# Optimization experiments

Measured on AMD Instinct MI355X. Metric: run time of the kernel, lower is better.

The kernel has to match this reference:

```python
import jax, jax.numpy as jnp
import numpy as np

NODE_DIM = 128
CAT = 16
N_NODES = 100000
N_EDGES = 200000
N_SCALARS = 6
INPUT_DIM = 5 * NODE_DIM + 5 * CAT + N_SCALARS  # 726
CELL_H, NET_H, OUT = 192, 128, 128
EPS = 1e-5


def setup_inputs() -> dict:
    key = jax.random.key(0)
    ks = jax.random.split(key, 24)
    inp = {
        'h_nodes': jax.random.normal(ks[0], (N_NODES, NODE_DIM), jnp.float32),
        'edge_scalars': jax.random.normal(ks[1], (N_EDGES, N_SCALARS), jnp.float32),
        'edge_src': jax.random.randint(ks[2], (N_EDGES,), 0, N_NODES),
        'edge_dst': jax.random.randint(ks[3], (N_EDGES,), 0, N_NODES),
        'edge_type': jax.random.randint(ks[4], (N_EDGES,), 0, 2),
        'cell_type_src': jax.random.randint(ks[5], (N_EDGES,), 0, 256),
        'cell_type_dst': jax.random.randint(ks[6], (N_EDGES,), 0, 256),
        'pin_role_src': jax.random.randint(ks[7], (N_EDGES,), 0, 64),
        'pin_role_dst': jax.random.randint(ks[8], (N_EDGES,), 0, 64),
        # embedding tables
        'emb_edge_type': jax.random.normal(ks[9], (2, CAT), jnp.float32),
        'emb_cell_type': jax.random.normal(ks[10], (256, CAT), jnp.float32),
        'emb_pin_role': jax.random.normal(ks[11], (64, CAT), jnp.float32),
        # cell MLP params
        'cell_W1': jax.random.normal(ks[12], (INPUT_DIM, CELL_H), jnp.float32) * (1.0 / np.sqrt(INPUT_DIM)),
        'cell_b1': jnp.zeros((CELL_H,), jnp.float32),
        'cell_g': jnp.ones((CELL_H,), jnp.float32),
        'cell_beta': jnp.zeros((CELL_H,), jnp.float32),
        'cell_W2': jax.random.normal(ks[13], (CELL_H, OUT), jnp.float32) * (1.0 / np.sqrt(CELL_H)),
        'cell_b2': jnp.zeros((OUT,), jnp.float32),
        # net MLP params
        'net_W1': jax.random.normal(ks[14], (INPUT_DIM, NET_H), jnp.float32) * (1.0 / np.sqrt(INPUT_DIM)),
        'net_b1': jnp.zeros((NET_H,), jnp.float32),
        'net_g': jnp.ones((NET_H,), jnp.float32),
        'net_beta': jnp.zeros((NET_H,), jnp.float32),
        'net_W2': jax.random.normal(ks[15], (NET_H, OUT), jnp.float32) * (1.0 / np.sqrt(NET_H)),
        'net_b2': jnp.zeros((OUT,), jnp.float32),
    }
    return inp


def _oov(x, n):
    return jnp.where((x >= 0) & (x < n), x, 0)


def _mlp(x, W1, b1, g, beta, W2, b2):
    h = x @ W1 + b1
    mu = jnp.mean(h, axis=-1, keepdims=True)
    var = jnp.mean(jnp.square(h - mu), axis=-1, keepdims=True)
    h = (h - mu) * jax.lax.rsqrt(var + EPS) * g + beta
    h = jax.nn.relu(h)
    return h @ W2 + b2


def reference(h_nodes, edge_scalars, emb_edge_type, emb_cell_type, emb_pin_role,
              cell_W1, cell_b1, cell_g, cell_beta, cell_W2, cell_b2,
              net_W1, net_b1, net_g, net_beta, net_W2, net_b2,
              edge_src, edge_dst, edge_type, cell_type_src, cell_type_dst,
              pin_role_src, pin_role_dst):
    h_u = h_nodes[edge_src]                      # [E, D]
    h_v = h_nodes[edge_dst]
    h_prod = h_u * h_v
    h_abs_diff = jnp.abs(h_u - h_v)
    h_signed_diff = h_v - h_u
    e_et = emb_edge_type[_oov(edge_type, emb_edge_type.shape[0])]
    e_ct_s = emb_cell_type[_oov(cell_type_src, emb_cell_type.shape[0])]
    e_ct_d = emb_cell_type[_oov(cell_type_dst, emb_cell_type.shape[0])]
    e_pr_s = emb_pin_role[_oov(pin_role_src, emb_pin_role.shape[0])]
    e_pr_d = emb_pin_role[_oov(pin_role_dst, emb_pin_role.shape[0])]
    scal = jnp.clip(edge_scalars, -10.0, 10.0)
    feat = jnp.concatenate([h_u, h_v, h_prod, h_abs_diff, h_signed_diff,
                            e_et, e_ct_s, e_ct_d, e_pr_s, e_pr_d, scal], axis=-1)  # [E, 726]
    out_cell = _mlp(feat, cell_W1, cell_b1, cell_g, cell_beta, cell_W2, cell_b2)
    out_net = _mlp(feat, net_W1, net_b1, net_g, net_beta, net_W2, net_b2)
    et = edge_type[:, None]
    h_edges = jnp.where(et == 0, out_cell, jnp.where(et == 1, out_net, jnp.zeros_like(out_cell)))
    return h_edges
```

## Files before the change

kernel.cpp:

```cpp
#include <hip/hip_runtime.h>

#define KPAD 736
#define KS   23
#define FPAD 744
#define BM   32

typedef short bfrag8 __attribute__((ext_vector_type(8)));
typedef float f32x4 __attribute__((ext_vector_type(4)));

__device__ __forceinline__ unsigned short f2bf(float f) {
  union { float f; unsigned u; } v; v.f = f;
  unsigned r = v.u + 0x7fffu + ((v.u >> 16) & 1u);
  return (unsigned short)(r >> 16);
}
__device__ __forceinline__ unsigned pk2(float a, float b) {
  return (unsigned)f2bf(a) | ((unsigned)f2bf(b) << 16);
}

struct SmemP2 {
  unsigned short hb[BM][200];
  float red[4][BM][2];
  float mu[BM];
  float rs[BM];
  float ot[BM][132];
};
struct alignas(16) Smem {
  union {
    unsigned short feat[BM][FPAD];
    SmemP2 p2;
  } u;
};

__global__ void prep_weights(const float* __restrict__ cW1, const float* __restrict__ nW1,
                             const float* __restrict__ cW2, const float* __restrict__ nW2,
                             unsigned short* __restrict__ w1c, unsigned short* __restrict__ w1n,
                             unsigned short* __restrict__ w2c, unsigned short* __restrict__ w2n,
                             int* __restrict__ cnt) {
  int i = blockIdx.x * blockDim.x + threadIdx.x;
  if (i == 0) { cnt[0] = 0; cnt[1] = 0; }
  const int T0 = 12 * KS * 512, T1 = 8 * KS * 512, T2 = 8 * 6 * 512, T3 = 8 * 4 * 512;
  const int tot = T0 + T1 + T2 + T3;
  for (; i < tot; i += gridDim.x * blockDim.x) {
    int idx = i;
    const float* src; unsigned short* dst; int N, Kreal, KSm, rel;
    if (idx < T0)              { src = cW1; dst = w1c; N = 192; Kreal = 726; KSm = KS; rel = idx; }
    else if ((idx -= T0) < T1) { src = nW1; dst = w1n; N = 128; Kreal = 726; KSm = KS; rel = idx; }
    else if ((idx -= T1) < T2) { src = cW2; dst = w2c; N = 128; Kreal = 192; KSm = 6;  rel = idx; }
    else { idx -= T2;            src = nW2; dst = w2n; N = 128; Kreal = 128; KSm = 4;  rel = idx; }
    int blk = rel >> 9, within = rel & 511;
    int l = within >> 3, e = within & 7;
    int n16 = blk / KSm, k32 = blk - n16 * KSm;
    int n = n16 * 16 + (l & 15);
    int k = k32 * 32 + ((l >> 4) * 8) + e;
    dst[rel] = f2bf(k < Kreal ? src[(size_t)k * N + n] : 0.f);
  }
}

__global__ void compact_edges(const int* __restrict__ et, int* __restrict__ cnt,
                              int* __restrict__ l0, int* __restrict__ l1,
                              float* __restrict__ out, int n) {
  int i = blockIdx.x * blockDim.x + threadIdx.x;
  for (; i < n; i += gridDim.x * blockDim.x) {
    int ty = et[i];
    if (ty == 0)      l0[atomicAdd(&cnt[0], 1)] = i;
    else if (ty == 1) l1[atomicAdd(&cnt[1], 1)] = i;
    else {
      float4 z = make_float4(0.f, 0.f, 0.f, 0.f);
      float4* po = (float4*)(out + (size_t)i * 128);
      #pragma unroll
      for (int j = 0; j < 32; ++j) po[j] = z;
    }
  }
}

template <int CH>
__device__ __forceinline__ void mlp_tile(
    Smem& sm, int tile, int c, const int* __restrict__ list,
    const float* __restrict__ h_nodes, const float* __restrict__ edge_scalars,
    const int* __restrict__ esrc, const int* __restrict__ edst,
    const int* __restrict__ et_, const int* __restrict__ cts, const int* __restrict__ ctd,
    const int* __restrict__ prs, const int* __restrict__ prd,
    const float* __restrict__ emb_et, const float* __restrict__ emb_ct, const float* __restrict__ emb_pr,
    const unsigned short* __restrict__ w1f, const unsigned short* __restrict__ w2f,
    const float* __restrict__ b1, const float* __restrict__ g,
    const float* __restrict__ beta, const float* __restrict__ b2,
    float* __restrict__ out)
{
  constexpr int NF  = CH / 64;
  constexpr int KS2 = CH / 32;
  const int t    = threadIdx.x;
  const int lane = t & 63;
  const int wid  = t >> 6;
  const int base = tile * BM;
  const int lrow = lane & 15;
  const int kq   = (lane >> 4) * 8;

  float b1v[NF], gv[NF], bev[NF];
  #pragma unroll
  for (int nf = 0; nf < NF; ++nf) {
    int n = wid * (NF * 16) + nf * 16 + lrow;
    b1v[nf] = b1[n]; gv[nf] = g[n]; bev[nf] = beta[n];
  }
  float b2v[2];
  #pragma unroll
  for (int nf = 0; nf < 2; ++nf) b2v[nf] = b2[wid * 32 + nf * 16 + lrow];

  {
    const int r = t >> 3, l8 = t & 7;
    const int eid = (base + r < c) ? list[base + r] : -1;
    if (eid >= 0) {
      const float* bu = h_nodes + (size_t)esrc[eid] * 128;
      const float* bv = h_nodes + (size_t)edst[eid] * 128;
      #pragma unroll
      for (int j = 0; j < 4; ++j) {
        const int d = (l8 + 8 * j) * 4;
        float4 uu = *(const float4*)(bu + d);
        float4 vv = *(const float4*)(bv + d);
        float ua[4] = {uu.x, uu.y, uu.z, uu.w};
        float va[4] = {vv.x, vv.y, vv.z, vv.w};
        uint2 w0 = make_uint2(pk2(ua[0], ua[1]), pk2(ua[2], ua[3]));
        uint2 w1_ = make_uint2(pk2(va[0], va[1]), pk2(va[2], va[3]));
        uint2 w2_ = make_uint2(pk2(ua[0] * va[0], ua[1] * va[1]), pk2(ua[2] * va[2], ua[3] * va[3]));
        uint2 w3_ = make_uint2(pk2(fabsf(ua[0] - va[0]), fabsf(ua[1] - va[1])),
                               pk2(fabsf(ua[2] - va[2]), fabsf(ua[3] - va[3])));
        uint2 w4_ = make_uint2(pk2(va[0] - ua[0], va[1] - ua[1]), pk2(va[2] - ua[2], va[3] - ua[3]));
        *(uint2*)&sm.u.feat[r][0 * 128 + d] = w0;
        *(uint2*)&sm.u.feat[r][1 * 128 + d] = w1_;
        *(uint2*)&sm.u.feat[r][2 * 128 + d] = w2_;
        *(uint2*)&sm.u.feat[r][3 * 128 + d] = w3_;
        *(uint2*)&sm.u.feat[r][4 * 128 + d] = w4_;
      }
    } else {
      uint2 z = make_uint2(0u, 0u);
      #pragma unroll
      for (int j = 0; j < 4; ++j) {
        const int d = (l8 + 8 * j) * 4;
        #pragma unroll
        for (int s = 0; s < 5; ++s) *(uint2*)&sm.u.feat[r][s * 128 + d] = z;
      }
    }
  }
  {
    const int rb = t & 31, eb = t >> 5;
    const int eid = (base + rb < c) ? list[base + rb] : -1;
    if (eid >= 0) {
      int i0 = et_[eid]; i0 = ((unsigned)i0 < 2u)   ? i0 : 0;
      int i1 = cts[eid]; i1 = ((unsigned)i1 < 256u) ? i1 : 0;
      int i2 = ctd[eid]; i2 = ((unsigned)i2 < 256u) ? i2 : 0;
      int i3 = prs[eid]; i3 = ((unsigned)i3 < 64u)  ? i3 : 0;
      int i4 = prd[eid]; i4 = ((unsigned)i4 < 64u)  ? i4 : 0;
      const float* tp0 = emb_et + i0 * 16;
      const float* tp1 = emb_ct + i1 * 16;
      const float* tp2 = emb_ct + i2 * 16;
      const float* tp3 = emb_pr + i3 * 16;
      const float* tp4 = emb_pr + i4 * 16;
      const float* tp5 = edge_scalars + (size_t)eid * 6;
      #pragma unroll
      for (int j = 0; j < 12; ++j) {
        int e = eb * 12 + j;
        int tbl = e >> 4, off = e & 15;
        float v;
        if      (tbl == 0) v = tp0[off];
        else if (tbl == 1) v = tp1[off];
        else if (tbl == 2) v = tp2[off];
        else if (tbl == 3) v = tp3[off];
        else if (tbl == 4) v = tp4[off];
        else v = (off < 6) ? fminf(fmaxf(tp5[off < 6 ? off : 0], -10.f), 10.f) : 0.f;
        sm.u.feat[rb][640 + e] = f2bf(v);
      }
    } else {
      #pragma unroll
      for (int j = 0; j < 12; ++j) sm.u.feat[rb][640 + eb * 12 + j] = 0;
    }
  }
  __syncthreads();

  f32x4 acc[2][NF];
  #pragma unroll
  for (int mf = 0; mf < 2; ++mf)
    #pragma unroll
    for (int nf = 0; nf < NF; ++nf) acc[mf][nf] = 0;

  const char* wb = (const char*)w1f + ((size_t)(wid * NF) * KS) * 1024 + (size_t)lane * 16;
  bfrag8 bc[NF];
  #pragma unroll
  for (int nf = 0; nf < NF; ++nf) bc[nf] = *(const bfrag8*)(wb + (size_t)nf * KS * 1024);
  #pragma unroll
  for (int k32 = 1; k32 < KS; ++k32) {
    bfrag8 bn[NF];
    #pragma unroll
    for (int nf = 0; nf < NF; ++nf)
      bn[nf] = *(const bfrag8*)(wb + ((size_t)nf * KS + k32) * 1024);
    bfrag8 a0 = *(const bfrag8*)&sm.u.feat[lrow][(k32 - 1) * 32 + kq];
    bfrag8 a1 = *(const bfrag8*)&sm.u.feat[16 + lrow][(k32 - 1) * 32 + kq];
    #pragma unroll
    for (int nf = 0; nf < NF; ++nf) {
      acc[0][nf] = __builtin_amdgcn_mfma_f32_16x16x32_bf16(a0, bc[nf], acc[0][nf], 0, 0, 0);
      acc[1][nf] = __builtin_amdgcn_mfma_f32_16x16x32_bf16(a1, bc[nf], acc[1][nf], 0, 0, 0);
    }
    #pragma unroll
    for (int nf = 0; nf < NF; ++nf) bc[nf] = bn[nf];
  }
  {
    bfrag8 a0 = *(const bfrag8*)&sm.u.feat[lrow][(KS - 1) * 32 + kq];
    bfrag8 a1 = *(const bfrag8*)&sm.u.feat[16 + lrow][(KS - 1) * 32 + kq];
    #pragma unroll
    for (int nf = 0; nf < NF; ++nf) {
      acc[0][nf] = __builtin_amdgcn_mfma_f32_16x16x32_bf16(a0, bc[nf], acc[0][nf], 0, 0, 0);
      acc[1][nf] = __builtin_amdgcn_mfma_f32_16x16x32_bf16(a1, bc[nf], acc[1][nf], 0, 0, 0);
    }
  }
  __syncthreads();

  float sum_[2][4], sq_[2][4];
  #pragma unroll
  for (int mf = 0; mf < 2; ++mf)
    #pragma unroll
    for (int rg = 0; rg < 4; ++rg) {
      float s = 0.f, q = 0.f;
      #pragma unroll
      for (int nf = 0; nf < NF; ++nf) {
        float val = acc[mf][nf][rg] + b1v[nf];
        acc[mf][nf][rg] = val;
        s += val; q += val * val;
      }
      sum_[mf][rg] = s; sq_[mf][rg] = q;
    }
  #pragma unroll
  for (int d = 1; d < 16; d <<= 1) {
    #pragma unroll
    for (int mf = 0; mf < 2; ++mf)
      #pragma unroll
      for (int rg = 0; rg < 4; ++rg) {
        sum_[mf][rg] += __shfl_xor(sum_[mf][rg], d);
        sq_[mf][rg]  += __shfl_xor(sq_[mf][rg], d);
      }
  }
  if (lrow == 0) {
    const int half = lane >> 4;
    #pragma unroll
    for (int mf = 0; mf < 2; ++mf)
      #pragma unroll
      for (int rg = 0; rg < 4; ++rg) {
        int row = mf * 16 + half * 4 + rg;
        sm.u.p2.red[wid][row][0] = sum_[mf][rg];
        sm.u.p2.red[wid][row][1] = sq_[mf][rg];
      }
  }
  __syncthreads();
  if (t < BM) {
    float ss = sm.u.p2.red[0][t][0] + sm.u.p2.red[1][t][0] + sm.u.p2.red[2][t][0] + sm.u.p2.red[3][t][0];
    float qq = sm.u.p2.red[0][t][1] + sm.u.p2.red[1][t][1] + sm.u.p2.red[2][t][1] + sm.u.p2.red[3][t][1];
    float muv = ss * (1.f / CH);
    float var = fmaxf(qq * (1.f / CH) - muv * muv, 0.f);
    sm.u.p2.mu[t] = muv;
    sm.u.p2.rs[t] = rsqrtf(var + 1e-5f);
  }
  __syncthreads();

  #pragma unroll
  for (int mf = 0; mf < 2; ++mf)
    #pragma unroll
    for (int rg = 0; rg < 4; ++rg) {
      int row = mf * 16 + (lane >> 4) * 4 + rg;
      float muv = sm.u.p2.mu[row], rsv = sm.u.p2.rs[row];
      #pragma unroll
      for (int nf = 0; nf < NF; ++nf) {
        float v = (acc[mf][nf][rg] - muv) * rsv * gv[nf] + bev[nf];
        sm.u.p2.hb[row][wid * (NF * 16) + nf * 16 + lrow] = f2bf(fmaxf(v, 0.f));
      }
    }
  __syncthreads();

  f32x4 acc2[2][2];
  #pragma unroll
  for (int mf = 0; mf < 2; ++mf) { acc2[mf][0] = 0; acc2[mf][1] = 0; }
  const char* wb2 = (const char*)w2f + ((size_t)(wid * 2) * KS2) * 1024 + (size_t)lane * 16;
  bfrag8 c0 = *(const bfrag8*)(wb2);
  bfrag8 c1 = *(const bfrag8*)(wb2 + (size_t)KS2 * 1024);
  #pragma unroll
  for (int k32 = 1; k32 < KS2; ++k32) {
    bfrag8 n0 = *(const bfrag8*)(wb2 + (size_t)k32 * 1024);
    bfrag8 n1 = *(const bfrag8*)(wb2 + ((size_t)KS2 + k32) * 1024);
    bfrag8 a0 = *(const bfrag8*)&sm.u.p2.hb[lrow][(k32 - 1) * 32 + kq];
    bfrag8 a1 = *(const bfrag8*)&sm.u.p2.hb[16 + lrow][(k32 - 1) * 32 + kq];
    acc2[0][0] = __builtin_amdgcn_mfma_f32_16x16x32_bf16(a0, c0, acc2[0][0], 0, 0, 0);
    acc2[1][0] = __builtin_amdgcn_mfma_f32_16x16x32_bf16(a1, c0, acc2[1][0], 0, 0, 0);
    acc2[0][1] = __builtin_amdgcn_mfma_f32_16x16x32_bf16(a0, c1, acc2[0][1], 0, 0, 0);
    acc2[1][1] = __builtin_amdgcn_mfma_f32_16x16x32_bf16(a1, c1, acc2[1][1], 0, 0, 0);
    c0 = n0; c1 = n1;
  }
  {
    bfrag8 a0 = *(const bfrag8*)&sm.u.p2.hb[lrow][(KS2 - 1) * 32 + kq];
    bfrag8 a1 = *(const bfrag8*)&sm.u.p2.hb[16 + lrow][(KS2 - 1) * 32 + kq];
    acc2[0][0] = __builtin_amdgcn_mfma_f32_16x16x32_bf16(a0, c0, acc2[0][0], 0, 0, 0);
    acc2[1][0] = __builtin_amdgcn_mfma_f32_16x16x32_bf16(a1, c0, acc2[1][0], 0, 0, 0);
    acc2[0][1] = __builtin_amdgcn_mfma_f32_16x16x32_bf16(a0, c1, acc2[0][1], 0, 0, 0);
    acc2[1][1] = __builtin_amdgcn_mfma_f32_16x16x32_bf16(a1, c1, acc2[1][1], 0, 0, 0);
  }

  #pragma unroll
  for (int nf2 = 0; nf2 < 2; ++nf2) {
    int n = wid * 32 + nf2 * 16 + lrow;
    float bb = b2v[nf2];
    #pragma unroll
    for (int mf = 0; mf < 2; ++mf)
      #pragma unroll
      for (int rg = 0; rg < 4; ++rg)
        sm.u.p2.ot[mf * 16 + (lane >> 4) * 4 + rg][n] = acc2[mf][nf2][rg] + bb;
  }
  __syncthreads();

  {
    const int r = t >> 3, l8 = t & 7;
    const int eid = (base + r < c) ? list[base + r] : -1;
    if (eid >= 0) {
      float4* po = (float4*)(out + (size_t)eid * 128 + l8 * 16);
      const float4* ps = (const float4*)&sm.u.p2.ot[r][l8 * 16];
      #pragma unroll
      for (int j = 0; j < 4; ++j) po[j] = ps[j];
    }
  }
}

struct Args {
  const float *h_nodes, *edge_scalars;
  const int *esrc, *edst, *et, *cts, *ctd, *prs, *prd;
  const float *emb_et, *emb_ct, *emb_pr;
  const unsigned short *w1c, *w2c;
  const float *cb1, *cg, *cbe, *cb2;
  const unsigned short *w1n, *w2n;
  const float *nb1, *ng, *nbe, *nb2;
  const int *cnt, *l0, *l1;
  float* out;
};

__global__ __launch_bounds__(256, 3) void edge_mlp_all(Args A) {
  __shared__ Smem sm;
  const int c0 = A.cnt[0];
  const int nb0 = (c0 + BM - 1) / BM;
  const int b = blockIdx.x;
  if (b < nb0) {
    mlp_tile<192>(sm, b, c0, A.l0, A.h_nodes, A.edge_scalars, A.esrc, A.edst, A.et,
                  A.cts, A.ctd, A.prs, A.prd, A.emb_et, A.emb_ct, A.emb_pr,
                  A.w1c, A.w2c, A.cb1, A.cg, A.cbe, A.cb2, A.out);
  } else {
    const int c1 = A.cnt[1];
    const int t2 = b - nb0;
    if (t2 * BM < c1)
      mlp_tile<128>(sm, t2, c1, A.l1, A.h_nodes, A.edge_scalars, A.esrc, A.edst, A.et,
                    A.cts, A.ctd, A.prs, A.prd, A.emb_et, A.emb_ct, A.emb_pr,
                    A.w1n, A.w2n, A.nb1, A.ng, A.nbe, A.nb2, A.out);
  }
}

extern "C" void kernel_launch(void* const* d_in, const int* in_sizes, int n_in,
                              void* d_out, int out_size, void* d_ws, size_t ws_size,
                              hipStream_t stream) {
  (void)n_in; (void)out_size; (void)ws_size;
  const float* h_nodes      = (const float*)d_in[0];
  const float* edge_scalars = (const float*)d_in[1];
  const int*   edge_src     = (const int*)d_in[2];
  const int*   edge_dst     = (const int*)d_in[3];
  const int*   edge_type    = (const int*)d_in[4];
  const int*   ct_s         = (const int*)d_in[5];
  const int*   ct_d         = (const int*)d_in[6];
  const int*   pr_s         = (const int*)d_in[7];
  const int*   pr_d         = (const int*)d_in[8];
  const float* emb_et       = (const float*)d_in[9];
  const float* emb_ct       = (const float*)d_in[10];
  const float* emb_pr       = (const float*)d_in[11];
  const float* cW1 = (const float*)d_in[12];
  const float* cb1 = (const float*)d_in[13];
  const float* cg  = (const float*)d_in[14];
  const float* cbe = (const float*)d_in[15];
  const float* cW2 = (const float*)d_in[16];
  const float* cb2 = (const float*)d_in[17];
  const float* nW1 = (const float*)d_in[18];
  const float* nb1 = (const float*)d_in[19];
  const float* ng  = (const float*)d_in[20];
  const float* nbe = (const float*)d_in[21];
  const float* nW2 = (const float*)d_in[22];
  const float* nb2 = (const float*)d_in[23];
  const int n_edges = in_sizes[2];
  float* out = (float*)d_out;

  char* ws = (char*)d_ws;
  int* cnt   = (int*)ws;
  int* list0 = (int*)(ws + 256);
  int* list1 = list0 + n_edges;
  size_t woff = (256 + (size_t)2 * n_edges * sizeof(int) + 255) & ~(size_t)255;
  unsigned short* w1c = (unsigned short*)(ws + woff);
  unsigned short* w1n = w1c + 12 * KS * 512;
  unsigned short* w2c = w1n + 8 * KS * 512;
  unsigned short* w2n = w2c + 8 * 6 * 512;

  prep_weights<<<1080, 256, 0, stream>>>(cW1, nW1, cW2, nW2, w1c, w1n, w2c, w2n, cnt);
  compact_edges<<<(n_edges + 255) / 256, 256, 0, stream>>>(edge_type, cnt, list0, list1, out, n_edges);

  Args A;
  A.h_nodes = h_nodes; A.edge_scalars = edge_scalars;
  A.esrc = edge_src; A.edst = edge_dst; A.et = edge_type;
  A.cts = ct_s; A.ctd = ct_d; A.prs = pr_s; A.prd = pr_d;
  A.emb_et = emb_et; A.emb_ct = emb_ct; A.emb_pr = emb_pr;
  A.w1c = w1c; A.w2c = w2c; A.cb1 = cb1; A.cg = cg; A.cbe = cbe; A.cb2 = cb2;
  A.w1n = w1n; A.w2n = w2n; A.nb1 = nb1; A.ng = ng; A.nbe = nbe; A.nb2 = nb2;
  A.cnt = cnt; A.l0 = list0; A.l1 = list1; A.out = out;

  const int nbAll = (n_edges + BM - 1) / BM + 2;
  edge_mlp_all<<<nbAll, 256, 0, stream>>>(A);
}
```

Measured before the change: 254.5 us.

## Use 64-edge tiles with 512 threads and pack per-edge records during compaction

Doubles the edge tile to 64 rows and uses 8 waves arranged as 4 M-slices by 2 N-halves, with a 3-deep register prefetch of W1 fragments. The compaction pass now writes an int4 record per edge holding src, dst, edge id and packed category indices, so the MLP kernel does one load instead of several scattered index loads. The output staging buffer is dropped in favour of direct stores from the accumulators. This raises shared memory per block and writes output with 16-float strided stores instead of float4 rows, which may hurt coalescing.

```diff
diff --git a/kernel.cpp b/kernel.cpp
--- a/kernel.cpp
+++ b/kernel.cpp
@@ -1,9 +1,9 @@
 #include <hip/hip_runtime.h>
 
-#define KPAD 736
 #define KS   23
 #define FPAD 744
-#define BM   32
+#define BM   64
+#define SMSZ (64*744*2)
 
 typedef short bfrag8 __attribute__((ext_vector_type(8)));
 typedef float f32x4 __attribute__((ext_vector_type(4)));
@@ -16,20 +16,6 @@
 __device__ __forceinline__ unsigned pk2(float a, float b) {
   return (unsigned)f2bf(a) | ((unsigned)f2bf(b) << 16);
 }
-
-struct SmemP2 {
-  unsigned short hb[BM][200];
-  float red[4][BM][2];
-  float mu[BM];
-  float rs[BM];
-  float ot[BM][132];
-};
-struct alignas(16) Smem {
-  union {
-    unsigned short feat[BM][FPAD];
-    SmemP2 p2;
-  } u;
-};
 
 __global__ void prep_weights(const float* __restrict__ cW1, const float* __restrict__ nW1,
                              const float* __restrict__ cW2, const float* __restrict__ nW2,
@@ -56,15 +42,25 @@
   }
 }
 
-__global__ void compact_edges(const int* __restrict__ et, int* __restrict__ cnt,
-                              int* __restrict__ l0, int* __restrict__ l1,
+__global__ void compact_edges(const int* __restrict__ et,
+                              const int* __restrict__ esrc, const int* __restrict__ edst,
+                              const int* __restrict__ cts, const int* __restrict__ ctd,
+                              const int* __restrict__ prs, const int* __restrict__ prd,
+                              int* __restrict__ cnt, int4* __restrict__ r0, int4* __restrict__ r1,
                               float* __restrict__ out, int n) {
   int i = blockIdx.x * blockDim.x + threadIdx.x;
   for (; i < n; i += gridDim.x * blockDim.x) {
     int ty = et[i];
-    if (ty == 0)      l0[atomicAdd(&cnt[0], 1)] = i;
-    else if (ty == 1) l1[atomicAdd(&cnt[1], 1)] = i;
-    else {
+    if (ty == 0 || ty == 1) {
+      int c1 = cts[i]; c1 = ((unsigned)c1 < 256u) ? c1 : 0;
+      int c2 = ctd[i]; c2 = ((unsigned)c2 < 256u) ? c2 : 0;
+      int p1 = prs[i]; p1 = ((unsigned)p1 < 64u)  ? p1 : 0;
+      int p2 = prd[i]; p2 = ((unsigned)p2 < 64u)  ? p2 : 0;
+      int4 rec; rec.x = esrc[i]; rec.y = edst[i]; rec.z = i;
+      rec.w = c1 | (c2 << 8) | (p1 << 16) | (p2 << 22);
+      if (ty == 0) r0[atomicAdd(&cnt[0], 1)] = rec;
+      else         r1[atomicAdd(&cnt[1], 1)] = rec;
+    } else {
       float4 z = make_float4(0.f, 0.f, 0.f, 0.f);
       float4* po = (float4*)(out + (size_t)i * 128);
       #pragma unroll
@@ -75,42 +71,50 @@
 
 template <int CH>
 __device__ __forceinline__ void mlp_tile(
-    Smem& sm, int tile, int c, const int* __restrict__ list,
+    char* smraw, int* sEid, int tile, int c, int etv,
+    const int4* __restrict__ rec,
     const float* __restrict__ h_nodes, const float* __restrict__ edge_scalars,
-    const int* __restrict__ esrc, const int* __restrict__ edst,
-    const int* __restrict__ et_, const int* __restrict__ cts, const int* __restrict__ ctd,
-    const int* __restrict__ prs, const int* __restrict__ prd,
     const float* __restrict__ emb_et, const float* __restrict__ emb_ct, const float* __restrict__ emb_pr,
     const unsigned short* __restrict__ w1f, const unsigned short* __restrict__ w2f,
     const float* __restrict__ b1, const float* __restrict__ g,
     const float* __restrict__ beta, const float* __restrict__ b2,
     float* __restrict__ out)
 {
-  constexpr int NF  = CH / 64;
-  constexpr int KS2 = CH / 32;
+  constexpr int NF  = CH / 32;
+  constexpr int CHP = CH + 8;
+  unsigned short (*feat)[FPAD] = (unsigned short (*)[FPAD])smraw;
+  unsigned short (*hb)[CHP]    = (unsigned short (*)[CHP])smraw;
+  float (*red)[64][2] = (float (*)[64][2])(smraw + 90112);
+  float (*murs)[2]    = (float (*)[2])(smraw + 94208);
+
   const int t    = threadIdx.x;
   const int lane = t & 63;
   const int wid  = t >> 6;
-  const int base = tile * BM;
+  const int mi   = wid & 3;
+  const int ni   = wid >> 2;
   const int lrow = lane & 15;
   const int kq   = (lane >> 4) * 8;
-
-  float b1v[NF], gv[NF], bev[NF];
+  const int base = tile * BM;
+
+  float b1r[NF], gr[NF], ber[NF];
   #pragma unroll
   for (int nf = 0; nf < NF; ++nf) {
-    int n = wid * (NF * 16) + nf * 16 + lrow;
-    b1v[nf] = b1[n]; gv[nf] = g[n]; bev[nf] = beta[n];
-  }
-  float b2v[2];
-  #pragma unroll
-  for (int nf = 0; nf < 2; ++nf) b2v[nf] = b2[wid * 32 + nf * 16 + lrow];
+    int ncol = ni * (CH / 2) + nf * 16 + lrow;
+    b1r[nf] = b1[ncol]; gr[nf] = g[ncol]; ber[nf] = beta[ncol];
+  }
+  float b2r[4];
+  #pragma unroll
+  for (int nf2 = 0; nf2 < 4; ++nf2) b2r[nf2] = b2[ni * 64 + nf2 * 16 + lrow];
 
   {
     const int r = t >> 3, l8 = t & 7;
-    const int eid = (base + r < c) ? list[base + r] : -1;
-    if (eid >= 0) {
-      const float* bu = h_nodes + (size_t)esrc[eid] * 128;
-      const float* bv = h_nodes + (size_t)edst[eid] * 128;
+    const int idx = base + r;
+    const bool valid = idx < c;
+    int4 q = rec[valid ? idx : (c - 1)];
+    if (l8 == 0) sEid[r] = valid ? q.z : -1;
+    if (valid) {
+      const float* bu = h_nodes + (size_t)q.x * 128;
+      const float* bv = h_nodes + (size_t)q.y * 128;
       #pragma unroll
       for (int j = 0; j < 4; ++j) {
         const int d = (l8 + 8 * j) * 4;
@@ -118,17 +122,17 @@
         float4 vv = *(const float4*)(bv + d);
         float ua[4] = {uu.x, uu.y, uu.z, uu.w};
         float va[4] = {vv.x, vv.y, vv.z, vv.w};
-        uint2 w0 = make_uint2(pk2(ua[0], ua[1]), pk2(ua[2], ua[3]));
-        uint2 w1_ = make_uint2(pk2(va[0], va[1]), pk2(va[2], va[3]));
-        uint2 w2_ = make_uint2(pk2(ua[0] * va[0], ua[1] * va[1]), pk2(ua[2] * va[2], ua[3] * va[3]));
-        uint2 w3_ = make_uint2(pk2(fabsf(ua[0] - va[0]), fabsf(ua[1] - va[1])),
-                               pk2(fabsf(ua[2] - va[2]), fabsf(ua[3] - va[3])));
-        uint2 w4_ = make_uint2(pk2(va[0] - ua[0], va[1] - ua[1]), pk2(va[2] - ua[2], va[3] - ua[3]));
-        *(uint2*)&sm.u.feat[r][0 * 128 + d] = w0;
-        *(uint2*)&sm.u.feat[r][1 * 128 + d] = w1_;
-        *(uint2*)&sm.u.feat[r][2 * 128 + d] = w2_;
-        *(uint2*)&sm.u.feat[r][3 * 128 + d] = w3_;
-        *(uint2*)&sm.u.feat[r][4 * 128 + d] = w4_;
+        uint2 s0 = make_uint2(pk2(ua[0], ua[1]), pk2(ua[2], ua[3]));
+        uint2 s1 = make_uint2(pk2(va[0], va[1]), pk2(va[2], va[3]));
+        uint2 s2 = make_uint2(pk2(ua[0] * va[0], ua[1] * va[1]), pk2(ua[2] * va[2], ua[3] * va[3]));
+        uint2 s3 = make_uint2(pk2(fabsf(ua[0] - va[0]), fabsf(ua[1] - va[1])),
+                              pk2(fabsf(ua[2] - va[2]), fabsf(ua[3] - va[3])));
+        uint2 s4 = make_uint2(pk2(va[0] - ua[0], va[1] - ua[1]), pk2(va[2] - ua[2], va[3] - ua[3]));
+        *(uint2*)&feat[r][0 * 128 + d] = s0;
+        *(uint2*)&feat[r][1 * 128 + d] = s1;
+        *(uint2*)&feat[r][2 * 128 + d] = s2;
+        *(uint2*)&feat[r][3 * 128 + d] = s3;
+        *(uint2*)&feat[r][4 * 128 + d] = s4;
       }
     } else {
       uint2 z = make_uint2(0u, 0u);
@@ -136,221 +140,180 @@
       for (int j = 0; j < 4; ++j) {
         const int d = (l8 + 8 * j) * 4;
         #pragma unroll
-        for (int s = 0; s < 5; ++s) *(uint2*)&sm.u.feat[r][s * 128 + d] = z;
+        for (int s = 0; s < 5; ++s) *(uint2*)&feat[r][s * 128 + d] = z;
       }
     }
   }
   {
-    const int rb = t & 31, eb = t >> 5;
-    const int eid = (base + rb < c) ? list[base + rb] : -1;
-    if (eid >= 0) {
-      int i0 = et_[eid]; i0 = ((unsigned)i0 < 2u)   ? i0 : 0;
-      int i1 = cts[eid]; i1 = ((unsigned)i1 < 256u) ? i1 : 0;
-      int i2 = ctd[eid]; i2 = ((unsigned)i2 < 256u) ? i2 : 0;
-      int i3 = prs[eid]; i3 = ((unsigned)i3 < 64u)  ? i3 : 0;
-      int i4 = prd[eid]; i4 = ((unsigned)i4 < 64u)  ? i4 : 0;
-      const float* tp0 = emb_et + i0 * 16;
-      const float* tp1 = emb_ct + i1 * 16;
-      const float* tp2 = emb_ct + i2 * 16;
-      const float* tp3 = emb_pr + i3 * 16;
-      const float* tp4 = emb_pr + i4 * 16;
-      const float* tp5 = edge_scalars + (size_t)eid * 6;
+    const int row = t & 63, eb = t >> 6;
+    const int idx = base + row;
+    const bool valid = idx < c;
+    int4 q = rec[valid ? idx : (c - 1)];
+    const int eid = q.z, pk = q.w;
+    const int c1 = pk & 255, c2 = (pk >> 8) & 255, p1 = (pk >> 16) & 63, p2 = (pk >> 22) & 63;
+    float vals[12];
+    if (valid) {
       #pragma unroll
       for (int j = 0; j < 12; ++j) {
-        int e = eb * 12 + j;
-        int tbl = e >> 4, off = e & 15;
+        int e = eb * 12 + j, tbl = e >> 4, off = e & 15;
         float v;
-        if      (tbl == 0) v = tp0[off];
-        else if (tbl == 1) v = tp1[off];
-        else if (tbl == 2) v = tp2[off];
-        else if (tbl == 3) v = tp3[off];
-        else if (tbl == 4) v = tp4[off];
-        else v = (off < 6) ? fminf(fmaxf(tp5[off < 6 ? off : 0], -10.f), 10.f) : 0.f;
-        sm.u.feat[rb][640 + e] = f2bf(v);
+        if      (tbl == 0) v = emb_et[etv * 16 + off];
+        else if (tbl == 1) v = emb_ct[c1 * 16 + off];
+        else if (tbl == 2) v = emb_ct[c2 * 16 + off];
+        else if (tbl == 3) v = emb_pr[p1 * 16 + off];
+        else if (tbl == 4) v = emb_pr[p2 * 16 + off];
+        else v = (off < 6) ? fminf(fmaxf(edge_scalars[(size_t)eid * 6 + off], -10.f), 10.f) : 0.f;
+        vals[j] = v;
       }
     } else {
       #pragma unroll
-      for (int j = 0; j < 12; ++j) sm.u.feat[rb][640 + eb * 12 + j] = 0;
-    }
-  }
-  __syncthreads();
-
-  f32x4 acc[2][NF];
-  #pragma unroll
-  for (int mf = 0; mf < 2; ++mf)
-    #pragma unroll
-    for (int nf = 0; nf < NF; ++nf) acc[mf][nf] = 0;
-
-  const char* wb = (const char*)w1f + ((size_t)(wid * NF) * KS) * 1024 + (size_t)lane * 16;
-  bfrag8 bc[NF];
-  #pragma unroll
-  for (int nf = 0; nf < NF; ++nf) bc[nf] = *(const bfrag8*)(wb + (size_t)nf * KS * 1024);
-  #pragma unroll
-  for (int k32 = 1; k32 < KS; ++k32) {
-    bfrag8 bn[NF];
+      for (int j = 0; j < 12; ++j) vals[j] = 0.f;
+    }
+    uint2 w0 = make_uint2(pk2(vals[0], vals[1]), pk2(vals[2], vals[3]));
+    uint2 w1_ = make_uint2(pk2(vals[4], vals[5]), pk2(vals[6], vals[7]));
+    uint2 w2_ = make_uint2(pk2(vals[8], vals[9]), pk2(vals[10], vals[11]));
+    *(uint2*)&feat[row][640 + eb * 12 + 0] = w0;
+    *(uint2*)&feat[row][640 + eb * 12 + 4] = w1_;
+    *(uint2*)&feat[row][640 + eb * 12 + 8] = w2_;
+  }
+  __syncthreads();
+
+  f32x4 acc1[NF];
+  #pragma unroll
+  for (int nf = 0; nf < NF; ++nf) acc1[nf] = 0;
+  const unsigned short* wb = w1f + ((size_t)ni * NF * KS) * 512 + (size_t)lane * 8;
+  bfrag8 br[3][NF];
+  #pragma unroll
+  for (int nf = 0; nf < NF; ++nf) {
+    br[0][nf] = *(const bfrag8*)(wb + ((size_t)nf * KS + 0) * 512);
+    br[1][nf] = *(const bfrag8*)(wb + ((size_t)nf * KS + 1) * 512);
+  }
+  #pragma unroll
+  for (int k = 0; k < KS; ++k) {
+    if (k + 2 < KS) {
+      #pragma unroll
+      for (int nf = 0; nf < NF; ++nf)
+        br[(k + 2) % 3][nf] = *(const bfrag8*)(wb + ((size_t)nf * KS + (k + 2)) * 512);
+    }
+    bfrag8 a = *(const bfrag8*)&feat[mi * 16 + lrow][k * 32 + kq];
     #pragma unroll
     for (int nf = 0; nf < NF; ++nf)
-      bn[nf] = *(const bfrag8*)(wb + ((size_t)nf * KS + k32) * 1024);
-    bfrag8 a0 = *(const bfrag8*)&sm.u.feat[lrow][(k32 - 1) * 32 + kq];
-    bfrag8 a1 = *(const bfrag8*)&sm.u.feat[16 + lrow][(k32 - 1) * 32 + kq];
+      acc1[nf] = __builtin_amdgcn_mfma_f32_16x16x32_bf16(a, br[k % 3][nf], acc1[nf], 0, 0, 0);
+  }
+  __syncthreads();
+
+  float sums[4], sqs[4];
+  #pragma unroll
+  for (int rg = 0; rg < 4; ++rg) {
+    float s = 0.f, qd = 0.f;
     #pragma unroll
     for (int nf = 0; nf < NF; ++nf) {
-      acc[0][nf] = __builtin_amdgcn_mfma_f32_16x16x32_bf16(a0, bc[nf], acc[0][nf], 0, 0, 0);
-      acc[1][nf] = __builtin_amdgcn_mfma_f32_16x16x32_bf16(a1, bc[nf], acc[1][nf], 0, 0, 0);
-    }
-    #pragma unroll
-    for (int nf = 0; nf < NF; ++nf) bc[nf] = bn[nf];
-  }
-  {
-    bfrag8 a0 = *(const bfrag8*)&sm.u.feat[lrow][(KS - 1) * 32 + kq];
-    bfrag8 a1 = *(const bfrag8*)&sm.u.feat[16 + lrow][(KS - 1) * 32 + kq];
+      float v = acc1[nf][rg] + b1r[nf];
+      acc1[nf][rg] = v;
+      s += v; qd += v * v;
+    }
+    sums[rg] = s; sqs[rg] = qd;
+  }
+  #pragma unroll
+  for (int d = 1; d < 16; d <<= 1) {
+    #pragma unroll
+    for (int rg = 0; rg < 4; ++rg) {
+      sums[rg] += __shfl_xor(sums[rg], d);
+      sqs[rg]  += __shfl_xor(sqs[rg], d);
+    }
+  }
+  if (lrow == 0) {
+    const int qr = lane >> 4;
+    #pragma unroll
+    for (int rg = 0; rg < 4; ++rg) {
+      int row = mi * 16 + qr * 4 + rg;
+      red[ni][row][0] = sums[rg];
+      red[ni][row][1] = sqs[rg];
+    }
+  }
+  __syncthreads();
+  if (t < 64) {
+    float ss = red[0][t][0] + red[1][t][0];
+    float qq = red[0][t][1] + red[1][t][1];
+    float m = ss * (1.f / CH);
+    float va = fmaxf(qq * (1.f / CH) - m * m, 0.f);
+    murs[t][0] = m;
+    murs[t][1] = rsqrtf(va + 1e-5f);
+  }
+  __syncthreads();
+
+  #pragma unroll
+  for (int rg = 0; rg < 4; ++rg) {
+    int row = mi * 16 + (lane >> 4) * 4 + rg;
+    float m = murs[row][0], rv = murs[row][1];
     #pragma unroll
     for (int nf = 0; nf < NF; ++nf) {
-      acc[0][nf] = __builtin_amdgcn_mfma_f32_16x16x32_bf16(a0, bc[nf], acc[0][nf], 0, 0, 0);
-      acc[1][nf] = __builtin_amdgcn_mfma_f32_16x16x32_bf16(a1, bc[nf], acc[1][nf], 0, 0, 0);
-    }
-  }
-  __syncthreads();
-
-  float sum_[2][4], sq_[2][4];
-  #pragma unroll
-  for (int mf = 0; mf < 2; ++mf)
-    #pragma unroll
-    for (int rg = 0; rg < 4; ++rg) {
-      float s = 0.f, q = 0.f;
-      #pragma unroll
-      for (int nf = 0; nf < NF; ++nf) {
-        float val = acc[mf][nf][rg] + b1v[nf];
-        acc[mf][nf][rg] = val;
-        s += val; q += val * val;
-      }
-      sum_[mf][rg] = s; sq_[mf][rg] = q;
-    }
-  #pragma unroll
-  for (int d = 1; d < 16; d <<= 1) {
-    #pragma unroll
-    for (int mf = 0; mf < 2; ++mf)
-      #pragma unroll
-      for (int rg = 0; rg < 4; ++rg) {
-        sum_[mf][rg] += __shfl_xor(sum_[mf][rg], d);
-        sq_[mf][rg]  += __shfl_xor(sq_[mf][rg], d);
-      }
-  }
-  if (lrow == 0) {
-    const int half = lane >> 4;
-    #pragma unroll
-    for (int mf = 0; mf < 2; ++mf)
-      #pragma unroll
-      for (int rg = 0; rg < 4; ++rg) {
-        int row = mf * 16 + half * 4 + rg;
-        sm.u.p2.red[wid][row][0] = sum_[mf][rg];
-        sm.u.p2.red[wid][row][1] = sq_[mf][rg];
-      }
-  }
-  __syncthreads();
-  if (t < BM) {
-    float ss = sm.u.p2.red[0][t][0] + sm.u.p2.red[1][t][0] + sm.u.p2.red[2][t][0] + sm.u.p2.red[3][t][0];
-    float qq = sm.u.p2.red[0][t][1] + sm.u.p2.red[1][t][1] + sm.u.p2.red[2][t][1] + sm.u.p2.red[3][t][1];
-    float muv = ss * (1.f / CH);
-    float var = fmaxf(qq * (1.f / CH) - muv * muv, 0.f);
-    sm.u.p2.mu[t] = muv;
-    sm.u.p2.rs[t] = rsqrtf(var + 1e-5f);
-  }
-  __syncthreads();
-
-  #pragma unroll
-  for (int mf = 0; mf < 2; ++mf)
-    #pragma unroll
-    for (int rg = 0; rg < 4; ++rg) {
-      int row = mf * 16 + (lane >> 4) * 4 + rg;
-      float muv = sm.u.p2.mu[row], rsv = sm.u.p2.rs[row];
-      #pragma unroll
-      for (int nf = 0; nf < NF; ++nf) {
-        float v = (acc[mf][nf][rg] - muv) * rsv * gv[nf] + bev[nf];
-        sm.u.p2.hb[row][wid * (NF * 16) + nf * 16 + lrow] = f2bf(fmaxf(v, 0.f));
-      }
-    }
-  __syncthreads();
-
-  f32x4 acc2[2][2];
-  #pragma unroll
-  for (int mf = 0; mf < 2; ++mf) { acc2[mf][0] = 0; acc2[mf][1] = 0; }
-  const char* wb2 = (const char*)w2f + ((size_t)(wid * 2) * KS2) * 1024 + (size_t)lane * 16;
-  bfrag8 c0 = *(const bfrag8*)(wb2);
-  bfrag8 c1 = *(const bfrag8*)(wb2 + (size_t)KS2 * 1024);
-  #pragma unroll
-  for (int k32 = 1; k32 < KS2; ++k32) {
-    bfrag8 n0 = *(const bfrag8*)(wb2 + (size_t)k32 * 1024);
-    bfrag8 n1 = *(const bfrag8*)(wb2 + ((size_t)KS2 + k32) * 1024);
-    bfrag8 a0 = *(const bfrag8*)&sm.u.p2.hb[lrow][(k32 - 1) * 32 + kq];
-    bfrag8 a1 = *(const bfrag8*)&sm.u.p2.hb[16 + lrow][(k32 - 1) * 32 + kq];
-    acc2[0][0] = __builtin_amdgcn_mfma_f32_16x16x32_bf16(a0, c0, acc2[0][0], 0, 0, 0);
-    acc2[1][0] = __builtin_amdgcn_mfma_f32_16x16x32_bf16(a1, c0, acc2[1][0], 0, 0, 0);
-    acc2[0][1] = __builtin_amdgcn_mfma_f32_16x16x32_bf16(a0, c1, acc2[0][1], 0, 0, 0);
-    acc2[1][1] = __builtin_amdgcn_mfma_f32_16x16x32_bf16(a1, c1, acc2[1][1], 0, 0, 0);
-    c0 = n0; c1 = n1;
-  }
-  {
-    bfrag8 a0 = *(const bfrag8*)&sm.u.p2.hb[lrow][(KS2 - 1) * 32 + kq];
-    bfrag8 a1 = *(const bfrag8*)&sm.u.p2.hb[16 + lrow][(KS2 - 1) * 32 + kq];
-    acc2[0][0] = __builtin_amdgcn_mfma_f32_16x16x32_bf16(a0, c0, acc2[0][0], 0, 0, 0);
-    acc2[1][0] = __builtin_amdgcn_mfma_f32_16x16x32_bf16(a1, c0, acc2[1][0], 0, 0, 0);
-    acc2[0][1] = __builtin_amdgcn_mfma_f32_16x16x32_bf16(a0, c1, acc2[0][1], 0, 0, 0);
-    acc2[1][1] = __builtin_amdgcn_mfma_f32_16x16x32_bf16(a1, c1, acc2[1][1], 0, 0, 0);
-  }
-
-  #pragma unroll
-  for (int nf2 = 0; nf2 < 2; ++nf2) {
-    int n = wid * 32 + nf2 * 16 + lrow;
-    float bb = b2v[nf2];
-    #pragma unroll
-    for (int mf = 0; mf < 2; ++mf)
-      #pragma unroll
-      for (int rg = 0; rg < 4; ++rg)
-        sm.u.p2.ot[mf * 16 + (lane >> 4) * 4 + rg][n] = acc2[mf][nf2][rg] + bb;
-  }
-  __syncthreads();
-
-  {
-    const int r = t >> 3, l8 = t & 7;
-    const int eid = (base + r < c) ? list[base + r] : -1;
+      float v = (acc1[nf][rg] - m) * rv * gr[nf] + ber[nf];
+      hb[row][ni * (CH / 2) + nf * 16 + lrow] = f2bf(fmaxf(v, 0.f));
+    }
+  }
+  __syncthreads();
+
+  f32x4 acc2[4];
+  #pragma unroll
+  for (int nf2 = 0; nf2 < 4; ++nf2) acc2[nf2] = 0;
+  const unsigned short* wb2 = w2f + ((size_t)ni * 4 * NF) * 512 + (size_t)lane * 8;
+  bfrag8 cr[NF][4];
+  #pragma unroll
+  for (int k2 = 0; k2 < NF; ++k2)
+    #pragma unroll
+    for (int nf2 = 0; nf2 < 4; ++nf2)
+      cr[k2][nf2] = *(const bfrag8*)(wb2 + ((size_t)nf2 * NF + k2) * 512);
+  #pragma unroll
+  for (int k2 = 0; k2 < NF; ++k2) {
+    bfrag8 a = *(const bfrag8*)&hb[mi * 16 + lrow][k2 * 32 + kq];
+    #pragma unroll
+    for (int nf2 = 0; nf2 < 4; ++nf2)
+      acc2[nf2] = __builtin_amdgcn_mfma_f32_16x16x32_bf16(a, cr[k2][nf2], acc2[nf2], 0, 0, 0);
+  }
+
+  #pragma unroll
+  for (int rg = 0; rg < 4; ++rg) {
+    int row = mi * 16 + (lane >> 4) * 4 + rg;
+    int eid = sEid[row];
     if (eid >= 0) {
-      float4* po = (float4*)(out + (size_t)eid * 128 + l8 * 16);
-      const float4* ps = (const float4*)&sm.u.p2.ot[r][l8 * 16];
-      #pragma unroll
-      for (int j = 0; j < 4; ++j) po[j] = ps[j];
+      float* po = out + (size_t)eid * 128 + ni * 64 + lrow;
+      #pragma unroll
+      for (int nf2 = 0; nf2 < 4; ++nf2)
+        po[nf2 * 16] = acc2[nf2][rg] + b2r[nf2];
     }
   }
 }
 
 struct Args {
   const float *h_nodes, *edge_scalars;
-  const int *esrc, *edst, *et, *cts, *ctd, *prs, *prd;
   const float *emb_et, *emb_ct, *emb_pr;
   const unsigned short *w1c, *w2c;
   const float *cb1, *cg, *cbe, *cb2;
   const unsigned short *w1n, *w2n;
   const float *nb1, *ng, *nbe, *nb2;
-  const int *cnt, *l0, *l1;
+  const int *cnt;
+  const int4 *r0, *r1;
   float* out;
 };
 
-__global__ __launch_bounds__(256, 3) void edge_mlp_all(Args A) {
-  __shared__ Smem sm;
+__global__ __launch_bounds__(512, 2) void edge_mlp_all(Args A) {
+  __shared__ char smraw[SMSZ];
+  __shared__ int sEid[64];
   const int c0 = A.cnt[0];
   const int nb0 = (c0 + BM - 1) / BM;
   const int b = blockIdx.x;
   if (b < nb0) {
-    mlp_tile<192>(sm, b, c0, A.l0, A.h_nodes, A.edge_scalars, A.esrc, A.edst, A.et,
-                  A.cts, A.ctd, A.prs, A.prd, A.emb_et, A.emb_ct, A.emb_pr,
-                  A.w1c, A.w2c, A.cb1, A.cg, A.cbe, A.cb2, A.out);
+    mlp_tile<192>(smraw, sEid, b, c0, 0, A.r0, A.h_nodes, A.edge_scalars,
+                  A.emb_et, A.emb_ct, A.emb_pr, A.w1c, A.w2c,
+                  A.cb1, A.cg, A.cbe, A.cb2, A.out);
   } else {
     const int c1 = A.cnt[1];
     const int t2 = b - nb0;
     if (t2 * BM < c1)
-      mlp_tile<128>(sm, t2, c1, A.l1, A.h_nodes, A.edge_scalars, A.esrc, A.edst, A.et,
-                    A.cts, A.ctd, A.prs, A.prd, A.emb_et, A.emb_ct, A.emb_pr,
-                    A.w1n, A.w2n, A.nb1, A.ng, A.nbe, A.nb2, A.out);
+      mlp_tile<128>(smraw, sEid, t2, c1, 1, A.r1, A.h_nodes, A.edge_scalars,
+                    A.emb_et, A.emb_ct, A.emb_pr, A.w1n, A.w2n,
+                    A.nb1, A.ng, A.nbe, A.nb2, A.out);
   }
 }
 
@@ -386,27 +349,27 @@
   float* out = (float*)d_out;
 
   char* ws = (char*)d_ws;
-  int* cnt   = (int*)ws;
-  int* list0 = (int*)(ws + 256);
-  int* list1 = list0 + n_edges;
-  size_t woff = (256 + (size_t)2 * n_edges * sizeof(int) + 255) & ~(size_t)255;
+  int* cnt = (int*)ws;
+  int4* r0 = (int4*)(ws + 256);
+  int4* r1 = r0 + n_edges;
+  size_t woff = (256 + (size_t)2 * n_edges * sizeof(int4) + 255) & ~(size_t)255;
   unsigned short* w1c = (unsigned short*)(ws + woff);
   unsigned short* w1n = w1c + 12 * KS * 512;
   unsigned short* w2c = w1n + 8 * KS * 512;
   unsigned short* w2n = w2c + 8 * 6 * 512;
 
   prep_weights<<<1080, 256, 0, stream>>>(cW1, nW1, cW2, nW2, w1c, w1n, w2c, w2n, cnt);
-  compact_edges<<<(n_edges + 255) / 256, 256, 0, stream>>>(edge_type, cnt, list0, list1, out, n_edges);
+  compact_edges<<<(n_edges + 255) / 256, 256, 0, stream>>>(edge_type, edge_src, edge_dst,
+                                                           ct_s, ct_d, pr_s, pr_d,
+                                                           cnt, r0, r1, out, n_edges);
 
   Args A;
   A.h_nodes = h_nodes; A.edge_scalars = edge_scalars;
-  A.esrc = edge_src; A.edst = edge_dst; A.et = edge_type;
-  A.cts = ct_s; A.ctd = ct_d; A.prs = pr_s; A.prd = pr_d;
   A.emb_et = emb_et; A.emb_ct = emb_ct; A.emb_pr = emb_pr;
   A.w1c = w1c; A.w2c = w2c; A.cb1 = cb1; A.cg = cg; A.cbe = cbe; A.cb2 = cb2;
   A.w1n = w1n; A.w2n = w2n; A.nb1 = nb1; A.ng = ng; A.nbe = nbe; A.nb2 = nb2;
-  A.cnt = cnt; A.l0 = list0; A.l1 = list1; A.out = out;
+  A.cnt = cnt; A.r0 = r0; A.r1 = r1; A.out = out;
 
   const int nbAll = (n_edges + BM - 1) / BM + 2;
-  edge_mlp_all<<<nbAll, 256, 0, stream>>>(A);
-}
+  edge_mlp_all<<<nbAll, 512, 0, stream>>>(A);
+}
```

After: 333.4 us. 31.0% more time.
